# Kernel optimization log

Hardware: AMD Instinct MI355X
Metric: run time of the kernel (lower is better)

Reference implementation:

```python
import jax, jax.numpy as jnp
import numpy as np

HIDDEN = 768
HEAD = 64


def setup_inputs() -> dict:
    key = jax.random.key(0)
    ks = jax.random.split(key, 9)
    s = 1.0 / np.sqrt(HIDDEN)
    so = 1.0 / np.sqrt(HEAD)
    return {
        "x": jax.random.normal(ks[0], (4, 4096, HIDDEN), dtype=jnp.float32),
        "Wq": jax.random.uniform(ks[1], (HIDDEN, HEAD), jnp.float32, -s, s),
        "bq": jax.random.uniform(ks[2], (HEAD,), jnp.float32, -s, s),
        "Wk": jax.random.uniform(ks[3], (HIDDEN, HEAD), jnp.float32, -s, s),
        "bk": jax.random.uniform(ks[4], (HEAD,), jnp.float32, -s, s),
        "Wv": jax.random.uniform(ks[5], (HIDDEN, HEAD), jnp.float32, -s, s),
        "bv": jax.random.uniform(ks[6], (HEAD,), jnp.float32, -s, s),
        "Wo": jax.random.uniform(ks[7], (HEAD, HIDDEN), jnp.float32, -so, so),
        "bo": jax.random.uniform(ks[8], (HIDDEN,), jnp.float32, -so, so),
    }


def reference(x, Wq, bq, Wk, bk, Wv, bv, Wo, bo):
    # x: [b, s, h]
    q = jnp.einsum('bsh,hd->bsd', x, Wq) + bq  # [b, s, d]
    k = jnp.einsum('bsh,hd->bsd', x, Wk) + bk
    v = jnp.einsum('bsh,hd->bsd', x, Wv) + bv
    scale = 1.0 / jnp.sqrt(jnp.asarray(HEAD, x.dtype))
    scores = jnp.einsum('bqd,bkd->bqk', q, k) * scale  # [b, s, s]
    A = jax.nn.softmax(scores, axis=-1)
    ctx = jnp.einsum('bqk,bkd->bqd', A, v)  # [b, s, d]
    return jnp.einsum('bsd,dh->bsh', ctx, Wo) + bo
```

## Files before the change

kernel.cpp:

```cpp
#include <hip/hip_runtime.h>
#include <hip/hip_bf16.h>
#include <stdint.h>

#define BB 4
#define SS 4096
#define HH 768
#define DD 64

typedef __attribute__((ext_vector_type(8))) short bf16x8;
typedef __attribute__((ext_vector_type(4))) short bf16x4;
typedef __attribute__((ext_vector_type(4))) float f32x4;
typedef __attribute__((ext_vector_type(16))) float f32x16;
typedef __attribute__((ext_vector_type(4))) uint32_t u32x4;

__device__ __forceinline__ short f2bf(float f) {
  uint32_t u = __builtin_bit_cast(uint32_t, f);
  u += 0x7fffu + ((u >> 16) & 1u);
  return (short)(u >> 16);
}

#define QSCALE 0.18033688011112042f

__global__ __launch_bounds__(256) void prep_kernel(
    const float* __restrict__ Wq, const float* __restrict__ bq,
    const float* __restrict__ Wk, const float* __restrict__ bk,
    const float* __restrict__ Wv, const float* __restrict__ bv,
    const float* __restrict__ Wo,
    short* __restrict__ wqkvF, float* __restrict__ bqkv,
    short* __restrict__ woF) {
  int idx = blockIdx.x * 256 + threadIdx.x;
  const int N1 = 192 * HH;
  const int N2 = HH * DD;
  if (idx < N1) {
    int n = idx / HH, k = idx % HH;
    float v;
    if (n < 64)       v = Wq[k * 64 + n] * QSCALE;
    else if (n < 128) v = Wk[k * 64 + (n - 64)];
    else              v = Wv[k * 64 + (n - 128)];
    int tile = (n >> 4) * 24 + (k >> 5);
    int lane = (((k >> 3) & 3) << 4) | (n & 15);
    wqkvF[tile * 512 + lane * 8 + (k & 7)] = f2bf(v);
  } else if (idx < N1 + N2) {
    int j = idx - N1;
    int n = j / 64, k = j % 64;
    int tile = (n >> 4) * 2 + (k >> 5);
    int lane = (((k >> 3) & 3) << 4) | (n & 15);
    woF[tile * 512 + lane * 8 + (k & 7)] = f2bf(Wo[k * HH + n]);
  } else if (idx < N1 + N2 + 192) {
    int n = idx - N1 - N2;
    float v;
    if (n < 64)       v = bq[n] * QSCALE;
    else if (n < 128) v = bk[n - 64];
    else              v = bv[n - 128];
    bqkv[n] = v;
  }
}

__global__ __launch_bounds__(256, 2) void qkv_kernel(
    const float* __restrict__ x, const short* __restrict__ wF,
    const float* __restrict__ bqkv,
    short* __restrict__ qb, short* __restrict__ kb, short* __restrict__ vb) {
  __shared__ short xl[32 * 776];
  const int tid = threadIdx.x;
  const int w = tid >> 6, lane = tid & 63, g = (lane >> 4) & 3, n16 = lane & 15;
  const int m0 = blockIdx.x * 32;

  const float4* xsrc = (const float4*)&x[m0 * HH];
#pragma unroll
  for (int i = 0; i < 24; ++i) {
    int idx = i * 256 + tid;
    const float4 f = xsrc[idx];
    int elem = idx * 4;
    int row = elem / HH, col = elem % HH;
    bf16x4 p = { f2bf(f.x), f2bf(f.y), f2bf(f.z), f2bf(f.w) };
    *(bf16x4*)&xl[row * 776 + col] = p;
  }
  __syncthreads();

  f32x4 acc[2][3] = {};
  const short* wbase = &wF[w * 36864 + lane * 8];

#pragma unroll 2
  for (int kc = 0; kc < 24; ++kc) {
    const int ko = kc * 32 + g * 8;
    bf16x8 a0 = *(const bf16x8*)&xl[n16 * 776 + ko];
    bf16x8 a1 = *(const bf16x8*)&xl[(16 + n16) * 776 + ko];
    bf16x8 b0 = *(const bf16x8*)&wbase[kc * 512];
    bf16x8 b1 = *(const bf16x8*)&wbase[12288 + kc * 512];
    bf16x8 b2 = *(const bf16x8*)&wbase[24576 + kc * 512];
    acc[0][0] = __builtin_amdgcn_mfma_f32_16x16x32_bf16(a0, b0, acc[0][0], 0, 0, 0);
    acc[1][0] = __builtin_amdgcn_mfma_f32_16x16x32_bf16(a1, b0, acc[1][0], 0, 0, 0);
    acc[0][1] = __builtin_amdgcn_mfma_f32_16x16x32_bf16(a0, b1, acc[0][1], 0, 0, 0);
    acc[1][1] = __builtin_amdgcn_mfma_f32_16x16x32_bf16(a1, b1, acc[1][1], 0, 0, 0);
    acc[0][2] = __builtin_amdgcn_mfma_f32_16x16x32_bf16(a0, b2, acc[0][2], 0, 0, 0);
    acc[1][2] = __builtin_amdgcn_mfma_f32_16x16x32_bf16(a1, b2, acc[1][2], 0, 0, 0);
  }

#pragma unroll
  for (int ct = 0; ct < 3; ++ct) {
    int nG = w * 48 + ct * 16 + n16;
    float bias = bqkv[nG];
#pragma unroll
    for (int rt = 0; rt < 2; ++rt)
#pragma unroll
      for (int r = 0; r < 4; ++r) {
        int rowg = m0 + rt * 16 + g * 4 + r;
        short val = f2bf(acc[rt][ct][r] + bias);
        if (nG < 64)        qb[rowg * 64 + nG] = val;
        else if (nG < 128)  kb[rowg * 64 + (nG - 64)] = val;
        else                vb[rowg * 64 + (nG - 128)] = val;
      }
  }
}

__global__ __launch_bounds__(256) void vtrans_kernel(
    const short* __restrict__ vb, short* __restrict__ vT) {
  __shared__ short t[64][72];
  const int tid = threadIdx.x;
  const int b = blockIdx.x >> 6, st = blockIdx.x & 63;
  {
    int row = tid >> 2, off = (tid & 3) * 16;
    const short* src = &vb[(b * SS + st * 64 + row) * 64 + off];
    *(bf16x8*)&t[row][off]     = *(const bf16x8*)&src[0];
    *(bf16x8*)&t[row][off + 8] = *(const bf16x8*)&src[8];
  }
  __syncthreads();
  {
    int d = tid >> 2, soff = (tid & 3) * 16;
    bf16x8 o0, o1;
#pragma unroll
    for (int j = 0; j < 8; ++j) o0[j] = t[soff + j][d];
#pragma unroll
    for (int j = 0; j < 8; ++j) o1[j] = t[soff + 8 + j][d];
    short* dst = &vT[(b * 64 + d) * SS + st * 64 + soff];
    *(bf16x8*)&dst[0] = o0;
    *(bf16x8*)&dst[8] = o1;
  }
}

__global__ __launch_bounds__(256, 3) void flash_kernel(
    const short* __restrict__ qb, const short* __restrict__ kb,
    const short* __restrict__ vT,
    float* __restrict__ Opart, float* __restrict__ lpart) {
  __shared__ short Kl[128 * 72];
  __shared__ short Vl[64 * 136];
  __shared__ float l_lds[64];
  const int tid = threadIdx.x;
  const int w = tid >> 6, lane = tid & 63;
  const int m31 = lane & 31, h = lane >> 5;
  const int qt32 = w & 1, kh = w >> 1;
  const int part = blockIdx.x, rg = part >> 2, sp = part & 3;
  const int b = rg >> 6, qt = rg & 63;
  const short* qB = qb + (b * SS + qt * 64 + qt32 * 32) * DD;
  const short* kB = kb + (b * SS + sp * 1024) * DD;
  const short* vB = vT + b * DD * SS + sp * 1024;

  bf16x8 aQ[4];
#pragma unroll
  for (int kk = 0; kk < 4; ++kk)
    aQ[kk] = *(const bf16x8*)&qB[m31 * DD + kk * 16 + 8 * h];

  f32x16 oacc[2] = {};
  float l_run = 0.f;

  for (int kt = 0; kt < 8; ++kt) {
    __syncthreads();
#pragma unroll
    for (int i = 0; i < 4; ++i) {
      int lin = tid + 256 * i;
      int key = lin >> 3, ch = lin & 7;
      *(bf16x8*)&Kl[key * 72 + ch * 8] =
          *(const bf16x8*)&kB[(kt * 128 + key) * DD + ch * 8];
    }
#pragma unroll
    for (int i = 0; i < 4; ++i) {
      int lin = tid + 256 * i;
      int d = lin >> 4, ch = lin & 15;
      *(bf16x8*)&Vl[d * 136 + ch * 8] =
          *(const bf16x8*)&vB[d * SS + kt * 128 + ch * 8];
    }
    __syncthreads();

#pragma unroll
    for (int kt2 = 0; kt2 < 2; ++kt2) {
      f32x16 sc = {};
#pragma unroll
      for (int kk = 0; kk < 4; ++kk) {
        bf16x8 aK = *(const bf16x8*)&Kl[(kh * 64 + kt2 * 32 + m31) * 72 +
                                        kk * 16 + 8 * h];
        sc = __builtin_amdgcn_mfma_f32_32x32x16_bf16(aK, aQ[kk], sc, 0, 0, 0);
      }

      uint32_t pp[8];
      float lsum = 0.f;
#pragma unroll
      for (int j = 0; j < 8; ++j) {
        uint32_t ta = __builtin_bit_cast(uint32_t,
                        __builtin_amdgcn_exp2f(sc[2 * j])) & 0xffff0000u;
        uint32_t tb = __builtin_bit_cast(uint32_t,
                        __builtin_amdgcn_exp2f(sc[2 * j + 1])) & 0xffff0000u;
        lsum += __builtin_bit_cast(float, ta) + __builtin_bit_cast(float, tb);
        pp[j] = (ta >> 16) | tb;
      }
      l_run += lsum;

      uint32_t ee[8];
#pragma unroll
      for (int j = 0; j < 8; ++j)
        ee[j] = (uint32_t)__shfl_xor((int)pp[j], 32);

#pragma unroll
      for (int s = 0; s < 2; ++s) {
        u32x4 fr;
        if (s == 0)
          fr = h ? u32x4{ee[2], ee[3], pp[2], pp[3]}
                 : u32x4{pp[0], pp[1], ee[0], ee[1]};
        else
          fr = h ? u32x4{ee[6], ee[7], pp[6], pp[7]}
                 : u32x4{pp[4], pp[5], ee[4], ee[5]};
        bf16x8 aP = __builtin_bit_cast(bf16x8, fr);
        const int koff = kh * 64 + kt2 * 32 + s * 16 + 8 * h;
#pragma unroll
        for (int dt = 0; dt < 2; ++dt) {
          bf16x8 bV = *(const bf16x8*)&Vl[(dt * 32 + m31) * 136 + koff];
          oacc[dt] = __builtin_amdgcn_mfma_f32_32x32x16_bf16(aP, bV, oacc[dt], 0, 0, 0);
        }
      }
    }
  }

  l_run += __shfl_xor(l_run, 32);

  __syncthreads();
  float* sO = (float*)Kl;
  if (kh == 1) {
#pragma unroll
    for (int dt = 0; dt < 2; ++dt)
#pragma unroll
      for (int r = 0; r < 16; ++r) {
        int q = (r & 3) + 8 * (r >> 2) + 4 * h;
        sO[qt32 * 2048 + q * 64 + dt * 32 + m31] = oacc[dt][r];
      }
    if (lane < 32) l_lds[qt32 * 32 + lane] = l_run;
  }
  __syncthreads();
  if (kh == 0) {
#pragma unroll
    for (int dt = 0; dt < 2; ++dt)
#pragma unroll
      for (int r = 0; r < 16; ++r) {
        int q = (r & 3) + 8 * (r >> 2) + 4 * h;
        float o = oacc[dt][r] + sO[qt32 * 2048 + q * 64 + dt * 32 + m31];
        Opart[(part * 64 + qt32 * 32 + q) * 64 + dt * 32 + m31] = o;
      }
    if (lane < 32)
      lpart[part * 64 + qt32 * 32 + lane] = l_run + l_lds[qt32 * 32 + lane];
  }
}

__global__ __launch_bounds__(256, 4) void proj_kernel(
    const float* __restrict__ Opart, const float* __restrict__ lpart,
    const short* __restrict__ woF, const float* __restrict__ bo,
    float* __restrict__ out) {
  const int tid = threadIdx.x;
  const int w = tid >> 6, lane = tid & 63, g = lane >> 4, n16 = lane & 15;
  const int m0 = blockIdx.x * 16;
  const int colbase = w * 192;

  const int row = m0 + n16;
  const int rg = row >> 6, r64 = row & 63;
  float lsum = lpart[(rg * 4 + 0) * 64 + r64] + lpart[(rg * 4 + 1) * 64 + r64] +
               lpart[(rg * 4 + 2) * 64 + r64] + lpart[(rg * 4 + 3) * 64 + r64];
  float inv = 1.f / lsum;

  bf16x8 aC[2];
#pragma unroll
  for (int kk = 0; kk < 2; ++kk) {
    const int d0 = kk * 32 + g * 8;
    float s0 = 0, s1 = 0, s2 = 0, s3 = 0, s4 = 0, s5 = 0, s6 = 0, s7 = 0;
#pragma unroll
    for (int sp = 0; sp < 4; ++sp) {
      const float* op = &Opart[((rg * 4 + sp) * 64 + r64) * 64 + d0];
      const float4 v0 = *(const float4*)&op[0];
      const float4 v1 = *(const float4*)&op[4];
      s0 += v0.x; s1 += v0.y; s2 += v0.z; s3 += v0.w;
      s4 += v1.x; s5 += v1.y; s6 += v1.z; s7 += v1.w;
    }
    aC[kk] = bf16x8{ f2bf(s0 * inv), f2bf(s1 * inv), f2bf(s2 * inv), f2bf(s3 * inv),
                     f2bf(s4 * inv), f2bf(s5 * inv), f2bf(s6 * inv), f2bf(s7 * inv) };
  }

  const short* wbase = &woF[w * 12288 + lane * 8];

  f32x4 acc[12] = {};
#pragma unroll
  for (int kk = 0; kk < 2; ++kk) {
#pragma unroll
    for (int ct = 0; ct < 12; ++ct) {
      bf16x8 bW = *(const bf16x8*)&wbase[(ct * 2 + kk) * 512];
      acc[ct] = __builtin_amdgcn_mfma_f32_16x16x32_bf16(aC[kk], bW, acc[ct], 0, 0, 0);
    }
  }
#pragma unroll
  for (int ct = 0; ct < 12; ++ct) {
    int nG = colbase + ct * 16 + n16;
    float bias = bo[nG];
#pragma unroll
    for (int r = 0; r < 4; ++r) {
      int rowg = m0 + g * 4 + r;
      out[rowg * HH + nG] = acc[ct][r] + bias;
    }
  }
}

extern "C" void kernel_launch(void* const* d_in, const int* in_sizes, int n_in,
                              void* d_out, int out_size, void* d_ws, size_t ws_size,
                              hipStream_t stream) {
  const float* x  = (const float*)d_in[0];
  const float* Wq = (const float*)d_in[1];
  const float* bq = (const float*)d_in[2];
  const float* Wk = (const float*)d_in[3];
  const float* bk = (const float*)d_in[4];
  const float* Wv = (const float*)d_in[5];
  const float* bv = (const float*)d_in[6];
  const float* Wo = (const float*)d_in[7];
  const float* bo = (const float*)d_in[8];
  float* out = (float*)d_out;

  char* ws = (char*)d_ws;
  short* qb    = (short*)(ws + 0);
  short* kb    = (short*)(ws + (2u << 20));
  short* vb    = (short*)(ws + (4u << 20));
  short* vT    = (short*)(ws + (6u << 20));
  short* wqkvF = (short*)(ws + (8u << 20));
  short* woF   = (short*)(ws + (8u << 20) + 384 * 1024);
  float* bqkv  = (float*)(ws + (8u << 20) + 512 * 1024);
  float* lpart = (float*)(ws + (9u << 20));
  float* Opart = (float*)(ws + (10u << 20));

  hipLaunchKernelGGL(prep_kernel, dim3(769), dim3(256), 0, stream,
                     Wq, bq, Wk, bk, Wv, bv, Wo, wqkvF, bqkv, woF);
  hipLaunchKernelGGL(qkv_kernel, dim3(512), dim3(256), 0, stream,
                     x, wqkvF, bqkv, qb, kb, vb);
  hipLaunchKernelGGL(vtrans_kernel, dim3(256), dim3(256), 0, stream,
                     vb, vT);
  hipLaunchKernelGGL(flash_kernel, dim3(1024), dim3(256), 0, stream,
                     qb, kb, vT, Opart, lpart);
  hipLaunchKernelGGL(proj_kernel, dim3(1024), dim3(256), 0, stream,
                     Opart, lpart, woF, bo, out);
}
```

Before: 170.2 us.

## Fuse V transpose into QKV kernel and use async swizzled LDS loads in flash

```diff
diff --git a/kernel.cpp b/kernel.cpp
--- a/kernel.cpp
+++ b/kernel.cpp
@@ -12,6 +12,11 @@
 typedef __attribute__((ext_vector_type(4))) float f32x4;
 typedef __attribute__((ext_vector_type(16))) float f32x16;
 typedef __attribute__((ext_vector_type(4))) uint32_t u32x4;
+
+typedef const __attribute__((address_space(1))) uint32_t g_u32;
+typedef __attribute__((address_space(3))) uint32_t l_u32;
+#define ASYNC16(gp, lp) \
+  __builtin_amdgcn_global_load_lds((g_u32*)(gp), (l_u32*)(lp), 16, 0, 0)
 
 __device__ __forceinline__ short f2bf(float f) {
   uint32_t u = __builtin_bit_cast(uint32_t, f);
@@ -59,8 +64,9 @@
 __global__ __launch_bounds__(256, 2) void qkv_kernel(
     const float* __restrict__ x, const short* __restrict__ wF,
     const float* __restrict__ bqkv,
-    short* __restrict__ qb, short* __restrict__ kb, short* __restrict__ vb) {
+    short* __restrict__ qb, short* __restrict__ kb, short* __restrict__ vT) {
   __shared__ short xl[32 * 776];
+  __shared__ short vtile[64 * 32];
   const int tid = threadIdx.x;
   const int w = tid >> 6, lane = tid & 63, g = (lane >> 4) & 3, n16 = lane & 15;
   const int m0 = blockIdx.x * 32;
@@ -100,50 +106,42 @@
   for (int ct = 0; ct < 3; ++ct) {
     int nG = w * 48 + ct * 16 + n16;
     float bias = bqkv[nG];
-#pragma unroll
-    for (int rt = 0; rt < 2; ++rt)
-#pragma unroll
-      for (int r = 0; r < 4; ++r) {
-        int rowg = m0 + rt * 16 + g * 4 + r;
-        short val = f2bf(acc[rt][ct][r] + bias);
-        if (nG < 64)        qb[rowg * 64 + nG] = val;
-        else if (nG < 128)  kb[rowg * 64 + (nG - 64)] = val;
-        else                vb[rowg * 64 + (nG - 128)] = val;
-      }
-  }
-}
-
-__global__ __launch_bounds__(256) void vtrans_kernel(
-    const short* __restrict__ vb, short* __restrict__ vT) {
-  __shared__ short t[64][72];
-  const int tid = threadIdx.x;
-  const int b = blockIdx.x >> 6, st = blockIdx.x & 63;
-  {
-    int row = tid >> 2, off = (tid & 3) * 16;
-    const short* src = &vb[(b * SS + st * 64 + row) * 64 + off];
-    *(bf16x8*)&t[row][off]     = *(const bf16x8*)&src[0];
-    *(bf16x8*)&t[row][off + 8] = *(const bf16x8*)&src[8];
-  }
+    if (nG < 128) {
+#pragma unroll
+      for (int rt = 0; rt < 2; ++rt)
+#pragma unroll
+        for (int r = 0; r < 4; ++r) {
+          int rowg = m0 + rt * 16 + g * 4 + r;
+          short val = f2bf(acc[rt][ct][r] + bias);
+          if (nG < 64) qb[rowg * 64 + nG] = val;
+          else         kb[rowg * 64 + (nG - 64)] = val;
+        }
+    } else {
+      int d = nG - 128;
+#pragma unroll
+      for (int rt = 0; rt < 2; ++rt) {
+        bf16x4 p = { f2bf(acc[rt][ct][0] + bias), f2bf(acc[rt][ct][1] + bias),
+                     f2bf(acc[rt][ct][2] + bias), f2bf(acc[rt][ct][3] + bias) };
+        *(bf16x4*)&vtile[d * 32 + rt * 16 + g * 4] = p;
+      }
+    }
+  }
+
   __syncthreads();
   {
-    int d = tid >> 2, soff = (tid & 3) * 16;
-    bf16x8 o0, o1;
-#pragma unroll
-    for (int j = 0; j < 8; ++j) o0[j] = t[soff + j][d];
-#pragma unroll
-    for (int j = 0; j < 8; ++j) o1[j] = t[soff + 8 + j][d];
-    short* dst = &vT[(b * 64 + d) * SS + st * 64 + soff];
-    *(bf16x8*)&dst[0] = o0;
-    *(bf16x8*)&dst[8] = o1;
-  }
-}
-
-__global__ __launch_bounds__(256, 3) void flash_kernel(
+    int d = tid >> 2, part = tid & 3;
+    bf16x8 o = *(const bf16x8*)&vtile[d * 32 + part * 8];
+    int b = m0 >> 12;
+    *(bf16x8*)&vT[(b * 64 + d) * SS + (m0 & 4095) + part * 8] = o;
+  }
+}
+
+__global__ __launch_bounds__(256, 4) void flash_kernel(
     const short* __restrict__ qb, const short* __restrict__ kb,
     const short* __restrict__ vT,
     float* __restrict__ Opart, float* __restrict__ lpart) {
-  __shared__ short Kl[128 * 72];
-  __shared__ short Vl[64 * 136];
+  __shared__ short Kl[128 * 64];
+  __shared__ short Vl[64 * 128];
   __shared__ float l_lds[64];
   const int tid = threadIdx.x;
   const int w = tid >> 6, lane = tid & 63;
@@ -155,6 +153,15 @@
   const short* kB = kb + (b * SS + sp * 1024) * DD;
   const short* vB = vT + b * DD * SS + sp * 1024;
 
+  int srcK[4], srcV[4];
+#pragma unroll
+  for (int i = 0; i < 4; ++i) {
+    int rowK = (w * 4 + i) * 8 + (lane >> 3);
+    srcK[i] = rowK * 64 + (((lane & 7) ^ (rowK & 7)) << 3);
+    int dV = (w * 4 + i) * 4 + (lane >> 4);
+    srcV[i] = dV * SS + (((lane & 15) ^ (dV & 15)) << 3);
+  }
+
   bf16x8 aQ[4];
 #pragma unroll
   for (int kk = 0; kk < 4; ++kk)
@@ -167,29 +174,23 @@
     __syncthreads();
 #pragma unroll
     for (int i = 0; i < 4; ++i) {
-      int lin = tid + 256 * i;
-      int key = lin >> 3, ch = lin & 7;
-      *(bf16x8*)&Kl[key * 72 + ch * 8] =
-          *(const bf16x8*)&kB[(kt * 128 + key) * DD + ch * 8];
-    }
-#pragma unroll
-    for (int i = 0; i < 4; ++i) {
-      int lin = tid + 256 * i;
-      int d = lin >> 4, ch = lin & 15;
-      *(bf16x8*)&Vl[d * 136 + ch * 8] =
-          *(const bf16x8*)&vB[d * SS + kt * 128 + ch * 8];
+      ASYNC16(kB + kt * 8192 + srcK[i], &Kl[(w * 4 + i) * 512]);
+      ASYNC16(vB + kt * 128  + srcV[i], &Vl[(w * 4 + i) * 512]);
     }
     __syncthreads();
 
 #pragma unroll
     for (int kt2 = 0; kt2 < 2; ++kt2) {
       f32x16 sc = {};
+      const int r = kh * 64 + kt2 * 32 + m31;
+      const int rx = r & 7;
+      __builtin_amdgcn_s_setprio(1);
 #pragma unroll
       for (int kk = 0; kk < 4; ++kk) {
-        bf16x8 aK = *(const bf16x8*)&Kl[(kh * 64 + kt2 * 32 + m31) * 72 +
-                                        kk * 16 + 8 * h];
+        bf16x8 aK = *(const bf16x8*)&Kl[r * 64 + ((((kk << 1) | h) ^ rx) << 3)];
         sc = __builtin_amdgcn_mfma_f32_32x32x16_bf16(aK, aQ[kk], sc, 0, 0, 0);
       }
+      __builtin_amdgcn_s_setprio(0);
 
       uint32_t pp[8];
       float lsum = 0.f;
@@ -219,12 +220,15 @@
           fr = h ? u32x4{ee[6], ee[7], pp[6], pp[7]}
                  : u32x4{pp[4], pp[5], ee[4], ee[5]};
         bf16x8 aP = __builtin_bit_cast(bf16x8, fr);
-        const int koff = kh * 64 + kt2 * 32 + s * 16 + 8 * h;
+        const int cv = (kh << 3) | (kt2 << 2) | (s << 1) | h;
+        __builtin_amdgcn_s_setprio(1);
 #pragma unroll
         for (int dt = 0; dt < 2; ++dt) {
-          bf16x8 bV = *(const bf16x8*)&Vl[(dt * 32 + m31) * 136 + koff];
+          const int rv = dt * 32 + m31;
+          bf16x8 bV = *(const bf16x8*)&Vl[rv * 128 + ((cv ^ (rv & 15)) << 3)];
           oacc[dt] = __builtin_amdgcn_mfma_f32_32x32x16_bf16(aP, bV, oacc[dt], 0, 0, 0);
         }
+        __builtin_amdgcn_s_setprio(0);
       }
     }
   }
@@ -330,20 +334,17 @@
   char* ws = (char*)d_ws;
   short* qb    = (short*)(ws + 0);
   short* kb    = (short*)(ws + (2u << 20));
-  short* vb    = (short*)(ws + (4u << 20));
-  short* vT    = (short*)(ws + (6u << 20));
-  short* wqkvF = (short*)(ws + (8u << 20));
-  short* woF   = (short*)(ws + (8u << 20) + 384 * 1024);
-  float* bqkv  = (float*)(ws + (8u << 20) + 512 * 1024);
-  float* lpart = (float*)(ws + (9u << 20));
-  float* Opart = (float*)(ws + (10u << 20));
+  short* vT    = (short*)(ws + (4u << 20));
+  short* wqkvF = (short*)(ws + (6u << 20));
+  short* woF   = (short*)(ws + (6u << 20) + 384 * 1024);
+  float* bqkv  = (float*)(ws + (6u << 20) + 512 * 1024);
+  float* lpart = (float*)(ws + (7u << 20));
+  float* Opart = (float*)(ws + (8u << 20));
 
   hipLaunchKernelGGL(prep_kernel, dim3(769), dim3(256), 0, stream,
                      Wq, bq, Wk, bk, Wv, bv, Wo, wqkvF, bqkv, woF);
   hipLaunchKernelGGL(qkv_kernel, dim3(512), dim3(256), 0, stream,
-                     x, wqkvF, bqkv, qb, kb, vb);
-  hipLaunchKernelGGL(vtrans_kernel, dim3(256), dim3(256), 0, stream,
-                     vb, vT);
+                     x, wqkvF, bqkv, qb, kb, vT);
   hipLaunchKernelGGL(flash_kernel, dim3(1024), dim3(256), 0, stream,
                      qb, kb, vT, Opart, lpart);
   hipLaunchKernelGGL(proj_kernel, dim3(1024), dim3(256), 0, stream,
```

Result: faster. 159.9 us (-6.1%).
